# Performance work log

Measured on AMD Instinct MI355X. Metric: run time of the kernel, lower is better.

Reference implementation:

```python
import jax, jax.numpy as jnp
import numpy as np

D_MODEL = 768
D_STATE = 16
D_CONV = 4
EXPAND = 2
D_INNER = EXPAND * D_MODEL  # 1536
BATCH = 2
SEQLEN = 4096


def setup_inputs() -> dict:
    key = jax.random.key(0)
    ks = jax.random.split(key, 8)
    s = 0.02
    return {
        "hidden_states": jax.random.normal(ks[0], (BATCH, SEQLEN, D_MODEL), jnp.float32),
        "W_in": jax.random.normal(ks[1], (D_MODEL, 2 * D_INNER), jnp.float32) * s,
        "conv_w": jax.random.normal(ks[2], (D_INNER, 1, D_CONV), jnp.float32) * s,
        "conv_b": jnp.zeros((D_INNER,), jnp.float32),
        "W_x": jax.random.normal(ks[3], (D_INNER, 2 * D_STATE + D_INNER), jnp.float32) * s,
        "W_dt": jax.random.normal(ks[4], (D_INNER, D_INNER), jnp.float32) * s,
        "b_dt": jnp.zeros((D_INNER,), jnp.float32),
        "A_log": jax.random.uniform(ks[5], (D_INNER, D_STATE), jnp.float32, minval=-1.0, maxval=0.0),
        "D": jnp.ones((D_INNER,), jnp.float32),
        "W_out": jax.random.normal(ks[6], (D_INNER, D_MODEL), jnp.float32) * s,
    }


def _silu(x):
    return x * jax.nn.sigmoid(x)


def reference(hidden_states, W_in, conv_w, conv_b, W_x, W_dt, b_dt, A_log, D, W_out):
    B, L, _ = hidden_states.shape
    # in_proj and split into x / gate z  (torch splits first half -> x, second -> z)
    xz = hidden_states @ W_in                      # (B, L, 2*ed)
    x, z = xz[..., :D_INNER], xz[..., D_INNER:]
    # causal depthwise conv1d (torch pads d_conv-1 both sides then truncates to L == left pad)
    xc = jnp.swapaxes(x, 1, 2)                     # (B, ed, L)
    xc = jax.lax.conv_general_dilated(
        xc, conv_w, window_strides=(1,), padding=[(D_CONV - 1, 0)],
        dimension_numbers=("NCH", "OIH", "NCH"), feature_group_count=D_INNER)
    x = jnp.swapaxes(xc, 1, 2) + conv_b            # (B, L, ed)
    x = _silu(x)
    # input-dependent SSM params
    xp = x @ W_x                                   # (B, L, 2*ds + ed)
    Bm = jax.nn.softmax(xp[..., :D_STATE], axis=-1)          # (B, L, ds)
    Cm = xp[..., D_STATE:2 * D_STATE]                          # (B, L, ds)
    delta = jax.nn.softplus(xp[..., 2 * D_STATE:] @ W_dt + b_dt)  # (B, L, ed)
    A = -jnp.exp(A_log.astype(jnp.float32))        # (ed, ds)

    def step(h, t):
        dt, Bt, Ct, ut = t                         # (B,ed),(B,ds),(B,ds),(B,ed)
        dA = jnp.exp(dt[:, :, None] * A)           # (B, ed, ds)
        h = dA * h + (dt[:, :, None] * Bt[:, None, :]) * ut[:, :, None]
        y = jnp.einsum('bs,bds->bd', Ct, h)        # (B, ed)
        return h, y

    h0 = jnp.zeros((B, D_INNER, D_STATE), x.dtype)
    ts = (jnp.swapaxes(delta, 0, 1), jnp.swapaxes(Bm, 0, 1),
          jnp.swapaxes(Cm, 0, 1), jnp.swapaxes(x, 0, 1))
    _, ys = jax.lax.scan(step, h0, ts)             # ys: (L, B, ed)
    y = jnp.swapaxes(ys, 0, 1)                     # (B, L, ed)
    # gating + out projection (torch fallback path does NOT add D * u)
    y = y * _silu(z)
    return y @ W_out
```

## Files before the change

### kernel.cpp

```cpp
#include <hip/hip_runtime.h>
#include <hip/hip_bf16.h>
#include <math.h>

#define D_MODEL 768
#define D_STATE 16
#define D_CONVW 4
#define D_INNER 1536
#define BATCH   2
#define SEQLEN  4096
#define NROWS   (BATCH*SEQLEN)
#define NCHUNK  128
#define LCHUNK  (SEQLEN/NCHUNK)

typedef __attribute__((ext_vector_type(8))) short short8;
typedef __attribute__((ext_vector_type(4))) float floatx4;

__device__ inline unsigned short f2b(float x) {
    unsigned u = __float_as_uint(x);
    return (unsigned short)((u + 0x7fffu + ((u >> 16) & 1u)) >> 16);
}
__device__ inline float b2f(unsigned short b) {
    return __uint_as_float(((unsigned)b) << 16);
}

#define GLDS(gp, lp) __builtin_amdgcn_global_load_lds( \
    (const __attribute__((address_space(1))) void*)(gp), \
    (__attribute__((address_space(3))) void*)(lp), 16, 0, 0)


template<int EPI, int OUTBF16>
__global__ __launch_bounds__(512, 4) void gemm_w8(
    const unsigned short* __restrict__ A, int lda,
    const unsigned short* __restrict__ Bt, int ldb,
    void* __restrict__ Cv, int ldc, float* __restrict__ C2,
    int N, int K, const float* __restrict__ bias, int nbx)
{
    __shared__ unsigned short As0[256*32], As1[256*32];
    __shared__ unsigned short Bs0[128*32], Bs1[128*32];

    const int nwg = gridDim.x;
    const int cpx = nwg >> 3;
    const int wg  = blockIdx.x;
    const int xcd = wg & 7, local = wg >> 3;
    int bmi, bni;
    if ((cpx % nbx == 0) && ((nbx & 1) == 0)) {
        const int R   = cpx / nbx;
        const int p   = local / (2 * R);
        const int idx = local % (2 * R);
        bmi = xcd * R + (idx >> 1);
        bni = p * 2 + (idx & 1);
    } else {
        const int swz = xcd * cpx + local;
        bmi = swz / nbx;
        bni = swz % nbx;
    }
    const int bm = bmi * 256;
    const int bn = bni * 128;

    const int tid  = threadIdx.x;
    const int lane = tid & 63;
    const int wave = tid >> 6;
    const int wm   = (wave >> 1) * 64;
    const int wn   = (wave & 1) * 64;
    const int l15  = lane & 15;
    const int lg   = lane >> 4;

    const int sr    = tid >> 2;
    const int sg    = ((tid & 3) ^ ((tid >> 3) & 3)) * 8;
    const int lbase = (tid & ~63) * 16;

    const unsigned short* pa0 = A  + (size_t)(bm + sr) * lda + sg;
    const unsigned short* pa1 = A  + (size_t)(bm + 128 + sr) * lda + sg;
    const unsigned short* pb0 = Bt + (size_t)(bn + sr) * ldb + sg;

    int aoff[4], boff[4];
    #pragma unroll
    for (int i = 0; i < 4; ++i) {
        const int tr = wm + i * 16 + l15;
        aoff[i] = tr * 64 + ((lg ^ ((tr >> 1) & 3)) << 4);
    }
    #pragma unroll
    for (int j = 0; j < 4; ++j) {
        const int tr = wn + j * 16 + l15;
        boff[j] = tr * 64 + ((lg ^ ((tr >> 1) & 3)) << 4);
    }

    floatx4 acc[4][4] = {};

    auto stage = [&](unsigned short (&SA)[256*32], unsigned short (&SB)[128*32]) {
        GLDS(pa0, (char*)SA + lbase);
        GLDS(pa1, (char*)SA + 8192 + lbase);
        GLDS(pb0, (char*)SB + lbase);
        pa0 += 32; pa1 += 32; pb0 += 32;
    };

    auto compute = [&](const unsigned short (&CA)[256*32],
                       const unsigned short (&CB)[128*32]) {
        short8 af[4], bfv[4];
        #pragma unroll
        for (int i = 0; i < 4; ++i)
            af[i] = *(const short8*)((const char*)&CA[0] + aoff[i]);
        #pragma unroll
        for (int j = 0; j < 4; ++j)
            bfv[j] = *(const short8*)((const char*)&CB[0] + boff[j]);
        #pragma unroll
        for (int i = 0; i < 4; ++i)
            #pragma unroll
            for (int j = 0; j < 4; ++j)
                acc[i][j] = __builtin_amdgcn_mfma_f32_16x16x32_bf16(
                    af[i], bfv[j], acc[i][j], 0, 0, 0);
    };

    const int NT = K >> 5;

    stage(As0, Bs0);

    #define STEP(SA, SB, CA, CB, T)                                          \
    {                                                                        \
        if ((T) + 1 < NT) {                                                  \
            stage(SA, SB);                                                   \
            asm volatile("s_waitcnt vmcnt(3)" ::: "memory");                 \
        } else {                                                             \
            asm volatile("s_waitcnt vmcnt(0)" ::: "memory");                 \
        }                                                                    \
        __builtin_amdgcn_sched_barrier(0);                                   \
        __builtin_amdgcn_s_barrier();                                        \
        __builtin_amdgcn_sched_barrier(0);                                   \
        compute(CA, CB);                                                     \
        __builtin_amdgcn_sched_barrier(0);                                   \
        __builtin_amdgcn_s_barrier();                                        \
        __builtin_amdgcn_sched_barrier(0);                                   \
    }

    for (int t = 0; t < NT; t += 2) {
        STEP(As1, Bs1, As0, Bs0, t);
        STEP(As0, Bs0, As1, Bs1, t + 1);
    }
    #undef STEP

    #pragma unroll
    for (int i = 0; i < 4; ++i) {
        #pragma unroll
        for (int r = 0; r < 4; ++r) {
            const int gm = bm + wm + i * 16 + lg * 4 + r;
            #pragma unroll
            for (int j = 0; j < 4; ++j) {
                const int gn = bn + wn + j * 16 + l15;
                float v = acc[i][j][r];
                if (EPI == 3) {
                    if (gn < 32) {
                        C2[(size_t)gm * 32 + gn] = v;
                    } else if (gn < N) {
                        v += bias[gn - 32];
                        v = (v > 20.f) ? v : log1pf(__expf(v));
                        ((unsigned short*)Cv)[(size_t)gm * 1536 + gn - 32] = f2b(v);
                    }
                } else {
                    if (gn < N) {
                        if (OUTBF16)
                            ((unsigned short*)Cv)[(size_t)gm * ldc + gn] = f2b(v);
                        else
                            ((float*)Cv)[(size_t)gm * ldc + gn] = v;
                    }
                }
            }
        }
    }
}

template<int EPI, int OUTBF16>
__global__ __launch_bounds__(256, 4) void gemm_p2(
    const unsigned short* __restrict__ A, int lda,
    const unsigned short* __restrict__ Bt, int ldb,
    void* __restrict__ Cv, int ldc, float* __restrict__ C2,
    int N, int K, const float* __restrict__ bias, int nbx)
{
    __shared__ unsigned short As0[128*32], As1[128*32];
    __shared__ unsigned short Bs0[128*32], Bs1[128*32];

    const int nwg = gridDim.x;
    const int cpx = nwg >> 3;
    const int wg  = blockIdx.x;
    const int xcd = wg & 7, local = wg >> 3;
    int bmi, bni;
    if ((cpx % nbx == 0) && ((nbx & 1) == 0)) {
        const int R   = cpx / nbx;
        const int p   = local / (2 * R);
        const int idx = local % (2 * R);
        bmi = xcd * R + (idx >> 1);
        bni = p * 2 + (idx & 1);
    } else {
        const int swz = xcd * cpx + local;
        bmi = swz / nbx;
        bni = swz % nbx;
    }
    const int bm = bmi * 128;
    const int bn = bni * 128;

    const int tid  = threadIdx.x;
    const int lane = tid & 63;
    const int wave = tid >> 6;
    const int wm   = (wave >> 1) * 64;
    const int wn   = (wave & 1) * 64;
    const int l15  = lane & 15;
    const int lg   = lane >> 4;

    const int sr    = tid >> 2;
    const int sg    = ((tid & 3) ^ ((tid >> 3) & 3)) * 8;
    const int lbase = (tid & ~63) * 16;

    const unsigned short* pa0 = A  + (size_t)(bm + sr) * lda + sg;
    const unsigned short* pa1 = A  + (size_t)(bm + 64 + sr) * lda + sg;
    const unsigned short* pb0 = Bt + (size_t)(bn + sr) * ldb + sg;
    const unsigned short* pb1 = Bt + (size_t)(bn + 64 + sr) * ldb + sg;

    int aoff[4], boff[4];
    #pragma unroll
    for (int i = 0; i < 4; ++i) {
        const int tr = wm + i * 16 + l15;
        aoff[i] = tr * 64 + ((lg ^ ((tr >> 1) & 3)) << 4);
    }
    #pragma unroll
    for (int j = 0; j < 4; ++j) {
        const int tr = wn + j * 16 + l15;
        boff[j] = tr * 64 + ((lg ^ ((tr >> 1) & 3)) << 4);
    }

    floatx4 acc[4][4] = {};

    auto stage = [&](unsigned short (&SA)[128*32], unsigned short (&SB)[128*32]) {
        GLDS(pa0, (char*)SA + lbase);
        GLDS(pa1, (char*)SA + 4096 + lbase);
        GLDS(pb0, (char*)SB + lbase);
        GLDS(pb1, (char*)SB + 4096 + lbase);
        pa0 += 32; pa1 += 32; pb0 += 32; pb1 += 32;
    };

    auto compute = [&](const unsigned short (&CA)[128*32],
                       const unsigned short (&CB)[128*32]) {
        short8 af[4], bfv[4];
        #pragma unroll
        for (int i = 0; i < 4; ++i)
            af[i] = *(const short8*)((const char*)&CA[0] + aoff[i]);
        #pragma unroll
        for (int j = 0; j < 4; ++j)
            bfv[j] = *(const short8*)((const char*)&CB[0] + boff[j]);
        #pragma unroll
        for (int i = 0; i < 4; ++i)
            #pragma unroll
            for (int j = 0; j < 4; ++j)
                acc[i][j] = __builtin_amdgcn_mfma_f32_16x16x32_bf16(
                    af[i], bfv[j], acc[i][j], 0, 0, 0);
    };

    const int NT = K >> 5;

    stage(As0, Bs0);

    #define STEP(SA, SB, CA, CB, T)                                          \
    {                                                                        \
        if ((T) + 1 < NT) {                                                  \
            stage(SA, SB);                                                   \
            asm volatile("s_waitcnt vmcnt(4)" ::: "memory");                 \
        } else {                                                             \
            asm volatile("s_waitcnt vmcnt(0)" ::: "memory");                 \
        }                                                                    \
        __builtin_amdgcn_sched_barrier(0);                                   \
        __builtin_amdgcn_s_barrier();                                        \
        __builtin_amdgcn_sched_barrier(0);                                   \
        compute(CA, CB);                                                     \
        __builtin_amdgcn_sched_barrier(0);                                   \
        __builtin_amdgcn_s_barrier();                                        \
        __builtin_amdgcn_sched_barrier(0);                                   \
    }

    for (int t = 0; t < NT; t += 2) {
        STEP(As1, Bs1, As0, Bs0, t);
        STEP(As0, Bs0, As1, Bs1, t + 1);
    }
    #undef STEP

    #pragma unroll
    for (int i = 0; i < 4; ++i) {
        #pragma unroll
        for (int r = 0; r < 4; ++r) {
            const int gm = bm + wm + i * 16 + lg * 4 + r;
            #pragma unroll
            for (int j = 0; j < 4; ++j) {
                const int gn = bn + wn + j * 16 + l15;
                float v = acc[i][j][r];
                if (gn < N) {
                    if (OUTBF16)
                        ((unsigned short*)Cv)[(size_t)gm * ldc + gn] = f2b(v);
                    else
                        ((float*)Cv)[(size_t)gm * ldc + gn] = v;
                }
            }
        }
    }
}

__global__ __launch_bounds__(256) void transpose_bf16(
    const float* __restrict__ W, unsigned short* __restrict__ Wt, int K, int N)
{
    __shared__ float t[32][33];
    const int nt = blockIdx.x * 32, kt = blockIdx.y * 32;
    const int tx = threadIdx.x & 31, ty = threadIdx.x >> 5;
    #pragma unroll
    for (int r = 0; r < 4; ++r) {
        const int k = ty + r * 8;
        const int n = nt + tx;
        float v = 0.f;
        if (n < N) v = W[(size_t)(kt + k) * N + n];
        t[k][tx] = v;
    }
    __syncthreads();
    #pragma unroll
    for (int r = 0; r < 4; ++r) {
        const int nl = ty + r * 8;
        Wt[(size_t)(nt + nl) * K + kt + tx] = f2b(t[tx][nl]);
    }
}

__global__ __launch_bounds__(256) void f32_to_bf16(
    const float* __restrict__ in, unsigned short* __restrict__ o, int n4)
{
    const int i = blockIdx.x * 256 + threadIdx.x;
    if (i >= n4) return;
    float4 v = ((const float4*)in)[i];
    ushort4 r;
    r.x = f2b(v.x); r.y = f2b(v.y); r.z = f2b(v.z); r.w = f2b(v.w);
    ((ushort4*)o)[i] = r;
}

__global__ __launch_bounds__(256) void wx32_to_bf16(
    const float* __restrict__ Wx, unsigned short* __restrict__ o)
{
    const int i = blockIdx.x * 256 + threadIdx.x;
    if (i >= 1536 * 384) return;
    const int row = i / 384, q = i % 384;
    float4 v = *(const float4*)(Wx + (size_t)row * 1568 + 32 + q * 4);
    ushort4 r;
    r.x = f2b(v.x); r.y = f2b(v.y); r.z = f2b(v.z); r.w = f2b(v.w);
    *(ushort4*)(o + (size_t)row * 1536 + q * 4) = r;
}

__global__ __launch_bounds__(256) void conv_silu8(
    const unsigned short* __restrict__ xzb, const float* __restrict__ w,
    const float* __restrict__ cb, unsigned short* __restrict__ ub)
{
    const int i = blockIdx.x * 256 + threadIdx.x;
    if (i >= NROWS * 192) return;
    const int g   = i % 192;
    const int row = i / 192;
    const int l   = row % SEQLEN;
    const int d0  = g * 8;

    short8 xr[4];
    #pragma unroll
    for (int k = 0; k < 4; ++k) {
        const int ll = l - 3 + k;
        if (ll >= 0)
            xr[k] = *(const short8*)&xzb[(size_t)(row - 3 + k) * 3072 + d0];
        else
            xr[k] = short8{0,0,0,0,0,0,0,0};
    }
    unsigned short o[8];
    #pragma unroll
    for (int e = 0; e < 8; ++e) {
        float4 we = *(const float4*)&w[(d0 + e) * 4];
        float a = cb[d0 + e];
        a = fmaf(b2f((unsigned short)xr[0][e]), we.x, a);
        a = fmaf(b2f((unsigned short)xr[1][e]), we.y, a);
        a = fmaf(b2f((unsigned short)xr[2][e]), we.z, a);
        a = fmaf(b2f((unsigned short)xr[3][e]), we.w, a);
        o[e] = f2b(a / (1.f + __expf(-a)));
    }
    *(short8*)&ub[(size_t)row * 1536 + d0] = *(short8*)o;
}

__global__ __launch_bounds__(256) void softmax_bc_kernel(
    const float* __restrict__ xp32, float* __restrict__ Bsm, float* __restrict__ Csm)
{
    const int row = blockIdx.x * 256 + threadIdx.x;
    if (row >= NROWS) return;
    const float* p = xp32 + (size_t)row * 32;
    float v[16];
    #pragma unroll
    for (int q = 0; q < 4; ++q) {
        float4 t = *(const float4*)(p + q * 4);
        v[q*4+0]=t.x; v[q*4+1]=t.y; v[q*4+2]=t.z; v[q*4+3]=t.w;
    }
    float mx = v[0];
    #pragma unroll
    for (int s = 1; s < 16; ++s) mx = fmaxf(mx, v[s]);
    float sum = 0.f;
    #pragma unroll
    for (int s = 0; s < 16; ++s) { v[s] = __expf(v[s] - mx); sum += v[s]; }
    const float inv = 1.f / sum;
    float* bo = Bsm + (size_t)row * 16;
    float* co = Csm + (size_t)row * 16;
    #pragma unroll
    for (int s = 0; s < 16; ++s) bo[s] = v[s] * inv;
    #pragma unroll
    for (int q = 0; q < 4; ++q)
        *(float4*)(co + q * 4) = *(const float4*)(p + 16 + q * 4);
}

__global__ __launch_bounds__(256) void scan_chunk_state(
    const unsigned short* __restrict__ deltab, const unsigned short* __restrict__ ub,
    const float* __restrict__ Bsm, const float* __restrict__ A_log,
    float* __restrict__ chunkS, float* __restrict__ dtsum)
{
    const int gid = blockIdx.x * 256 + threadIdx.x;
    const int d = gid % D_INNER;
    const int c = (gid / D_INNER) % NCHUNK;
    const int b = gid / (D_INNER * NCHUNK);

    float A2[16];
    #pragma unroll
    for (int q = 0; q < 4; ++q) {
        float4 t = *(const float4*)(A_log + d * 16 + q * 4);
        A2[q*4+0] = -__expf(t.x) * 1.44269504089f;
        A2[q*4+1] = -__expf(t.y) * 1.44269504089f;
        A2[q*4+2] = -__expf(t.z) * 1.44269504089f;
        A2[q*4+3] = -__expf(t.w) * 1.44269504089f;
    }
    float h[16];
    #pragma unroll
    for (int s = 0; s < 16; ++s) h[s] = 0.f;
    float dts = 0.f;

    const int t0 = c * LCHUNK;
    for (int t = t0; t < t0 + LCHUNK; ++t) {
        const size_t rowoff = (size_t)b * SEQLEN + t;
        const float dt = b2f(deltab[rowoff * D_INNER + d]);
        const float uu = b2f(ub[rowoff * D_INNER + d]);
        const float du = dt * uu;
        dts += dt;
        const float4* Bp = (const float4*)(Bsm + rowoff * 16);
        float Bv[16];
        #pragma unroll
        for (int q = 0; q < 4; ++q) {
            float4 tb = Bp[q];
            Bv[q*4+0]=tb.x; Bv[q*4+1]=tb.y; Bv[q*4+2]=tb.z; Bv[q*4+3]=tb.w;
        }
        #pragma unroll
        for (int s = 0; s < 16; ++s) {
            const float dA = exp2f(dt * A2[s]);
            h[s] = fmaf(dA, h[s], du * Bv[s]);
        }
    }
    float* S = chunkS + (size_t)gid * 16;
    #pragma unroll
    for (int q = 0; q < 4; ++q)
        *(float4*)(S + q * 4) = make_float4(h[q*4+0], h[q*4+1], h[q*4+2], h[q*4+3]);
    dtsum[gid] = dts;
}

__global__ __launch_bounds__(256) void scan_chunk_scan(
    const float* __restrict__ A_log, const float* __restrict__ dtsum,
    float* __restrict__ chunkS)
{
    const int gid = blockIdx.x * 256 + threadIdx.x;
    if (gid >= BATCH * D_INNER * 16) return;
    const int s = gid % 16;
    const int d = (gid / 16) % D_INNER;
    const int b = gid / (16 * D_INNER);
    const float A2 = -__expf(A_log[d * 16 + s]) * 1.44269504089f;
    float hprev = 0.f;
    for (int c = 0; c < NCHUNK; ++c) {
        const size_t cidx = ((size_t)(b * NCHUNK + c) * D_INNER + d);
        const float P  = exp2f(A2 * dtsum[cidx]);
        const size_t idx = cidx * 16 + s;
        const float Sc = chunkS[idx];
        chunkS[idx] = hprev;
        hprev = fmaf(P, hprev, Sc);
    }
}

__global__ __launch_bounds__(256) void scan_output(
    const unsigned short* __restrict__ deltab, const unsigned short* __restrict__ ub,
    const float* __restrict__ Bsm, const float* __restrict__ Csm,
    const float* __restrict__ A_log, const float* __restrict__ chunkS,
    const unsigned short* __restrict__ xzb, unsigned short* __restrict__ yb)
{
    const int gid = blockIdx.x * 256 + threadIdx.x;
    const int d = gid % D_INNER;
    const int c = (gid / D_INNER) % NCHUNK;
    const int b = gid / (D_INNER * NCHUNK);

    float A2[16];
    #pragma unroll
    for (int q = 0; q < 4; ++q) {
        float4 t = *(const float4*)(A_log + d * 16 + q * 4);
        A2[q*4+0] = -__expf(t.x) * 1.44269504089f;
        A2[q*4+1] = -__expf(t.y) * 1.44269504089f;
        A2[q*4+2] = -__expf(t.z) * 1.44269504089f;
        A2[q*4+3] = -__expf(t.w) * 1.44269504089f;
    }
    float h[16];
    const float* S = chunkS + (size_t)gid * 16;
    #pragma unroll
    for (int q = 0; q < 4; ++q) {
        float4 t = *(const float4*)(S + q * 4);
        h[q*4+0]=t.x; h[q*4+1]=t.y; h[q*4+2]=t.z; h[q*4+3]=t.w;
    }

    const int t0 = c * LCHUNK;
    for (int t = t0; t < t0 + LCHUNK; ++t) {
        const size_t rowoff = (size_t)b * SEQLEN + t;
        const float dt = b2f(deltab[rowoff * D_INNER + d]);
        const float uu = b2f(ub[rowoff * D_INNER + d]);
        const float du = dt * uu;
        const float4* Bp = (const float4*)(Bsm + rowoff * 16);
        const float4* Cp = (const float4*)(Csm + rowoff * 16);
        float Bv[16], Cv[16];
        #pragma unroll
        for (int q = 0; q < 4; ++q) {
            float4 tb = Bp[q], tc = Cp[q];
            Bv[q*4+0]=tb.x; Bv[q*4+1]=tb.y; Bv[q*4+2]=tb.z; Bv[q*4+3]=tb.w;
            Cv[q*4+0]=tc.x; Cv[q*4+1]=tc.y; Cv[q*4+2]=tc.z; Cv[q*4+3]=tc.w;
        }
        float yv = 0.f;
        #pragma unroll
        for (int s = 0; s < 16; ++s) {
            const float dA = exp2f(dt * A2[s]);
            h[s] = fmaf(dA, h[s], du * Bv[s]);
            yv = fmaf(Cv[s], h[s], yv);
        }
        const float z = b2f(xzb[rowoff * (2 * D_INNER) + D_INNER + d]);
        const float sz = z / (1.f + __expf(-z));
        yb[rowoff * D_INNER + d] = f2b(yv * sz);
    }
}

extern "C" void kernel_launch(void* const* d_in, const int* in_sizes, int n_in,
                              void* d_out, int out_size, void* d_ws, size_t ws_size,
                              hipStream_t stream)
{
    const float* hs     = (const float*)d_in[0];
    const float* W_in   = (const float*)d_in[1];
    const float* conv_w = (const float*)d_in[2];
    const float* conv_b = (const float*)d_in[3];
    const float* W_x    = (const float*)d_in[4];
    const float* W_dt   = (const float*)d_in[5];
    const float* b_dt   = (const float*)d_in[6];
    const float* A_log  = (const float*)d_in[7];
    const float* W_out  = (const float*)d_in[9];
    float* out = (float*)d_out;

    char* w = (char*)d_ws;
    auto alloc = [&](size_t bytes) { char* p = w; w += (bytes + 255) & ~(size_t)255; return p; };
    float*          xp32   = (float*)alloc((size_t)NROWS * 32 * 4);
    unsigned short* deltab = (unsigned short*)alloc((size_t)NROWS * 1536 * 2);
    float*          Bsm    = (float*)alloc((size_t)NROWS * 16 * 4);
    float*          Csm    = (float*)alloc((size_t)NROWS * 16 * 4);
    float*          chunkS = (float*)alloc((size_t)BATCH * NCHUNK * D_INNER * 16 * 4);
    float*          dtsum  = (float*)alloc((size_t)BATCH * NCHUNK * D_INNER * 4);
    unsigned short* xzb    = (unsigned short*)alloc((size_t)NROWS * 3072 * 2);
    unsigned short* ub     = (unsigned short*)alloc((size_t)NROWS * 1536 * 2);
    unsigned short* yb     = (unsigned short*)alloc((size_t)NROWS * 1536 * 2);
    unsigned short* hsb    = (unsigned short*)alloc((size_t)NROWS * 768 * 2);
    unsigned short* Wt_in  = (unsigned short*)alloc((size_t)3072 * 768 * 2);
    unsigned short* Wt_x   = (unsigned short*)alloc((size_t)1792 * 1536 * 2);
    unsigned short* Wt_dt  = (unsigned short*)alloc((size_t)1536 * 1536 * 2);
    unsigned short* Wt_out = (unsigned short*)alloc((size_t)768 * 1536 * 2);
    unsigned short* wxb    = (unsigned short*)alloc((size_t)1536 * 1536 * 2);

    const dim3 blk(256);

    transpose_bf16<<<dim3(3072/32, 768/32),  blk, 0, stream>>>(W_in,  Wt_in,  768,  3072);
    transpose_bf16<<<dim3(1792/32, 1536/32), blk, 0, stream>>>(W_x,   Wt_x,   1536, 1568);
    transpose_bf16<<<dim3(1536/32, 1536/32), blk, 0, stream>>>(W_dt,  Wt_dt,  1536, 1536);
    transpose_bf16<<<dim3(768/32,  1536/32), blk, 0, stream>>>(W_out, Wt_out, 1536, 768);
    f32_to_bf16<<<(NROWS*768/4 + 255)/256, blk, 0, stream>>>(hs, hsb, NROWS*768/4);
    wx32_to_bf16<<<(1536*384 + 255)/256, blk, 0, stream>>>(W_x, wxb);

    gemm_p2<0,1><<<dim3(144), blk, 0, stream>>>(
        Wt_dt, 1536, wxb, 1536, Wt_x + (size_t)32 * 1536, 1536, nullptr,
        1536, 1536, nullptr, 12);

    gemm_w8<0,1><<<dim3(768), dim3(512), 0, stream>>>(
        hsb, 768, Wt_in, 768, xzb, 3072, nullptr, 3072, 768, nullptr, 24);

    conv_silu8<<<(NROWS*192)/256, blk, 0, stream>>>(xzb, conv_w, conv_b, ub);

    gemm_w8<3,0><<<dim3(416), dim3(512), 0, stream>>>(
        ub, 1536, Wt_x, 1536, deltab, 1536, xp32, 1568, 1536, b_dt, 13);

    softmax_bc_kernel<<<NROWS/256, blk, 0, stream>>>(xp32, Bsm, Csm);

    scan_chunk_state<<<(BATCH*NCHUNK*D_INNER)/256, blk, 0, stream>>>(
        deltab, ub, Bsm, A_log, chunkS, dtsum);
    scan_chunk_scan<<<(BATCH*D_INNER*16 + 255)/256, blk, 0, stream>>>(
        A_log, dtsum, chunkS);
    scan_output<<<(BATCH*NCHUNK*D_INNER)/256, blk, 0, stream>>>(
        deltab, ub, Bsm, Csm, A_log, chunkS, xzb, yb);

    gemm_p2<0,0><<<dim3(384), blk, 0, stream>>>(
        yb, 1536, Wt_out, 1536, out, 768, nullptr, 768, 1536, nullptr, 6);
}
```

Measured before the change: 445.3 us.

## Enlarge GEMM tiles to 256x256 with K=64 stages

Replaces the 256x128 GEMM tile with a 256x256 tile and a K-step of 64 in the two big GEMMs, with 8x4 accumulator fragments per wave. This raises arithmetic intensity and halves the workgroup count. It also restructures the double-buffer pipeline to issue the next stage before compute, waiting with vmcnt(0) after it. In exchange it uses 128KB of LDS and many more registers, so occupancy drops to 2 waves per SIMD. The smaller grid (384 and 224 workgroups) may also underfill the 256 CUs, and the 224-block one leaves some idle.

```diff
diff --git a/kernel.cpp b/kernel.cpp
--- a/kernel.cpp
+++ b/kernel.cpp
@@ -27,16 +27,15 @@
     (const __attribute__((address_space(1))) void*)(gp), \
     (__attribute__((address_space(3))) void*)(lp), 16, 0, 0)
 
-
 template<int EPI, int OUTBF16>
-__global__ __launch_bounds__(512, 4) void gemm_w8(
+__global__ __launch_bounds__(512, 2) void gemm_t256(
     const unsigned short* __restrict__ A, int lda,
     const unsigned short* __restrict__ Bt, int ldb,
     void* __restrict__ Cv, int ldc, float* __restrict__ C2,
     int N, int K, const float* __restrict__ bias, int nbx)
 {
-    __shared__ unsigned short As0[256*32], As1[256*32];
-    __shared__ unsigned short Bs0[128*32], Bs1[128*32];
+    __shared__ unsigned short As0[256*64], As1[256*64];
+    __shared__ unsigned short Bs0[256*64], Bs1[256*64];
 
     const int nwg = gridDim.x;
     const int cpx = nwg >> 3;
@@ -55,97 +54,95 @@
         bni = swz % nbx;
     }
     const int bm = bmi * 256;
-    const int bn = bni * 128;
+    const int bn = bni * 256;
 
     const int tid  = threadIdx.x;
     const int lane = tid & 63;
     const int wave = tid >> 6;
-    const int wm   = (wave >> 1) * 64;
-    const int wn   = (wave & 1) * 64;
+    const int wr   = wave >> 2;
+    const int wc   = wave & 3;
     const int l15  = lane & 15;
     const int lg   = lane >> 4;
 
-    const int sr    = tid >> 2;
-    const int sg    = ((tid & 3) ^ ((tid >> 3) & 3)) * 8;
-    const int lbase = (tid & ~63) * 16;
-
-    const unsigned short* pa0 = A  + (size_t)(bm + sr) * lda + sg;
-    const unsigned short* pa1 = A  + (size_t)(bm + 128 + sr) * lda + sg;
-    const unsigned short* pb0 = Bt + (size_t)(bn + sr) * ldb + sg;
-
-    int aoff[4], boff[4];
-    #pragma unroll
-    for (int i = 0; i < 4; ++i) {
-        const int tr = wm + i * 16 + l15;
-        aoff[i] = tr * 64 + ((lg ^ ((tr >> 1) & 3)) << 4);
+    const int srow = tid >> 3;
+    const int sgc  = ((tid & 7) ^ ((tid >> 3) & 7)) * 8;
+    const unsigned short* pa = A  + (size_t)(bm + srow) * lda + sgc;
+    const unsigned short* pb = Bt + (size_t)(bn + srow) * ldb + sgc;
+
+    int aoff[8], boff[4];
+    #pragma unroll
+    for (int i = 0; i < 8; ++i) {
+        const int row = wr * 128 + i * 16 + l15;
+        aoff[i] = row * 128 + ((lg ^ (l15 & 7)) << 4);
     }
     #pragma unroll
     for (int j = 0; j < 4; ++j) {
-        const int tr = wn + j * 16 + l15;
-        boff[j] = tr * 64 + ((lg ^ ((tr >> 1) & 3)) << 4);
-    }
-
-    floatx4 acc[4][4] = {};
-
-    auto stage = [&](unsigned short (&SA)[256*32], unsigned short (&SB)[128*32]) {
-        GLDS(pa0, (char*)SA + lbase);
-        GLDS(pa1, (char*)SA + 8192 + lbase);
-        GLDS(pb0, (char*)SB + lbase);
-        pa0 += 32; pa1 += 32; pb0 += 32;
+        const int row = wc * 64 + j * 16 + l15;
+        boff[j] = row * 128 + ((lg ^ (l15 & 7)) << 4);
+    }
+
+    floatx4 acc[8][4] = {};
+
+    auto stage = [&](unsigned short (&SA)[256*64], unsigned short (&SB)[256*64]) {
+        #pragma unroll
+        for (int q = 0; q < 4; ++q)
+            GLDS(pa + (size_t)q * 64 * lda, (char*)&SA[0] + q * 8192 + tid * 16);
+        #pragma unroll
+        for (int q = 0; q < 4; ++q)
+            GLDS(pb + (size_t)q * 64 * ldb, (char*)&SB[0] + q * 8192 + tid * 16);
+        pa += 64; pb += 64;
     };
 
-    auto compute = [&](const unsigned short (&CA)[256*32],
-                       const unsigned short (&CB)[128*32]) {
-        short8 af[4], bfv[4];
-        #pragma unroll
-        for (int i = 0; i < 4; ++i)
-            af[i] = *(const short8*)((const char*)&CA[0] + aoff[i]);
-        #pragma unroll
-        for (int j = 0; j < 4; ++j)
-            bfv[j] = *(const short8*)((const char*)&CB[0] + boff[j]);
-        #pragma unroll
-        for (int i = 0; i < 4; ++i)
+    auto compute = [&](const unsigned short (&CA)[256*64],
+                       const unsigned short (&CB)[256*64]) {
+        #pragma unroll
+        for (int kk = 0; kk < 2; ++kk) {
+            const int kx = kk << 6;
+            short8 af[8], bfv[4];
+            #pragma unroll
+            for (int i = 0; i < 8; ++i)
+                af[i] = *(const short8*)((const char*)&CA[0] + (aoff[i] ^ kx));
             #pragma unroll
             for (int j = 0; j < 4; ++j)
-                acc[i][j] = __builtin_amdgcn_mfma_f32_16x16x32_bf16(
-                    af[i], bfv[j], acc[i][j], 0, 0, 0);
+                bfv[j] = *(const short8*)((const char*)&CB[0] + (boff[j] ^ kx));
+            #pragma unroll
+            for (int i = 0; i < 8; ++i)
+                #pragma unroll
+                for (int j = 0; j < 4; ++j)
+                    acc[i][j] = __builtin_amdgcn_mfma_f32_16x16x32_bf16(
+                        af[i], bfv[j], acc[i][j], 0, 0, 0);
+        }
     };
 
-    const int NT = K >> 5;
+    const int NT = K >> 6;
 
     stage(As0, Bs0);
-
-    #define STEP(SA, SB, CA, CB, T)                                          \
-    {                                                                        \
-        if ((T) + 1 < NT) {                                                  \
-            stage(SA, SB);                                                   \
-            asm volatile("s_waitcnt vmcnt(3)" ::: "memory");                 \
-        } else {                                                             \
-            asm volatile("s_waitcnt vmcnt(0)" ::: "memory");                 \
-        }                                                                    \
-        __builtin_amdgcn_sched_barrier(0);                                   \
-        __builtin_amdgcn_s_barrier();                                        \
-        __builtin_amdgcn_sched_barrier(0);                                   \
-        compute(CA, CB);                                                     \
-        __builtin_amdgcn_sched_barrier(0);                                   \
-        __builtin_amdgcn_s_barrier();                                        \
-        __builtin_amdgcn_sched_barrier(0);                                   \
-    }
+    asm volatile("s_waitcnt vmcnt(0)" ::: "memory");
+    __builtin_amdgcn_s_barrier();
 
     for (int t = 0; t < NT; t += 2) {
-        STEP(As1, Bs1, As0, Bs0, t);
-        STEP(As0, Bs0, As1, Bs1, t + 1);
-    }
-    #undef STEP
-
-    #pragma unroll
-    for (int i = 0; i < 4; ++i) {
+        if (t + 1 < NT) stage(As1, Bs1);
+        compute(As0, Bs0);
+        asm volatile("s_waitcnt vmcnt(0)" ::: "memory");
+        __builtin_amdgcn_sched_barrier(0);
+        __builtin_amdgcn_s_barrier();
+        __builtin_amdgcn_sched_barrier(0);
+        if (t + 2 < NT) stage(As0, Bs0);
+        compute(As1, Bs1);
+        asm volatile("s_waitcnt vmcnt(0)" ::: "memory");
+        __builtin_amdgcn_sched_barrier(0);
+        __builtin_amdgcn_s_barrier();
+        __builtin_amdgcn_sched_barrier(0);
+    }
+
+    #pragma unroll
+    for (int i = 0; i < 8; ++i) {
         #pragma unroll
         for (int r = 0; r < 4; ++r) {
-            const int gm = bm + wm + i * 16 + lg * 4 + r;
+            const int gm = bm + wr * 128 + i * 16 + lg * 4 + r;
             #pragma unroll
             for (int j = 0; j < 4; ++j) {
-                const int gn = bn + wn + j * 16 + l15;
+                const int gn = bn + wc * 64 + j * 16 + l15;
                 float v = acc[i][j][r];
                 if (EPI == 3) {
                     if (gn < 32) {
@@ -581,13 +578,13 @@
         Wt_dt, 1536, wxb, 1536, Wt_x + (size_t)32 * 1536, 1536, nullptr,
         1536, 1536, nullptr, 12);
 
-    gemm_w8<0,1><<<dim3(768), dim3(512), 0, stream>>>(
-        hsb, 768, Wt_in, 768, xzb, 3072, nullptr, 3072, 768, nullptr, 24);
+    gemm_t256<0,1><<<dim3(384), dim3(512), 0, stream>>>(
+        hsb, 768, Wt_in, 768, xzb, 3072, nullptr, 3072, 768, nullptr, 12);
 
     conv_silu8<<<(NROWS*192)/256, blk, 0, stream>>>(xzb, conv_w, conv_b, ub);
 
-    gemm_w8<3,0><<<dim3(416), dim3(512), 0, stream>>>(
-        ub, 1536, Wt_x, 1536, deltab, 1536, xp32, 1568, 1536, b_dt, 13);
+    gemm_t256<3,0><<<dim3(224), dim3(512), 0, stream>>>(
+        ub, 1536, Wt_x, 1536, deltab, 1536, xp32, 1568, 1536, b_dt, 7);
 
     softmax_bc_kernel<<<NROWS/256, blk, 0, stream>>>(xp32, Bsm, Csm);
 
```

Result: slower. 532.3 us (+19.5%).
